# Kernel tuning notes

Hardware: AMD Instinct MI355X
Metric: run time of the kernel (lower is better)

## Reference

```python
import jax, jax.numpy as jnp
import numpy as np

B, N, C, H = 2, 2048, 768, 12
HD = C // H
SCALE = HD ** -0.5


def setup_inputs() -> dict:
    key = jax.random.key(0)
    k1, k2, k3, k4 = jax.random.split(key, 4)
    return {
        "x": jax.random.normal(k1, (B, N, C), dtype=jnp.float32),
        "qkv_w": jax.random.normal(k2, (3 * C, C), dtype=jnp.float32) * (C ** -0.5),
        "proj_w": jax.random.normal(k3, (C, C), dtype=jnp.float32) * (C ** -0.5),
        "proj_b": jax.random.normal(k4, (C,), dtype=jnp.float32) * 0.01,
    }


def reference(x, qkv_w, proj_w, proj_b):
    b, n, c = x.shape
    # qkv: Linear(dim, 3*dim, bias=False) -> (B,N,3,H,HD) -> per-tensor (B,H,N,HD)
    qkv = (x @ qkv_w.T).reshape(b, n, 3, H, HD)
    q, k, v = jnp.moveaxis(qkv, 2, 0)          # each (B,N,H,HD)
    q = q.transpose(0, 2, 1, 3)                # (B,H,N,HD)
    k = k.transpose(0, 2, 1, 3)
    v = v.transpose(0, 2, 1, 3)
    attn_logits = jnp.einsum("bhqd,bhkd->bhqk", q, k) * SCALE  # (B,H,N,N)
    attn = jax.nn.softmax(attn_logits, axis=-1)
    score = jnp.mean(attn, axis=1)             # (B,N,N) mean over heads
    # dropout p=0.0 -> identity
    out = jnp.einsum("bhqk,bhkd->bhqd", attn, v)  # (B,H,N,HD)
    out = out.transpose(0, 2, 1, 3).reshape(b, n, c)
    out = out @ proj_w.T + proj_b
    return out, score
```

## Files before the change

kernel.cpp:

```cpp
#include <hip/hip_runtime.h>
#include <cstddef>

typedef __attribute__((ext_vector_type(8))) short bf16x8;
typedef __attribute__((ext_vector_type(4))) float f32x4;

constexpr int Bb = 2, Nn = 2048, Cc = 768, Hh = 12, HDd = 64;
constexpr float QSCALE = 0.125f * 1.44269504088896340736f;

#define VMCNT(n) asm volatile("s_waitcnt vmcnt(" #n ")" ::: "memory")
#define SBAR() __builtin_amdgcn_s_barrier()

__device__ inline short f2bf(float f) {
  unsigned u = __builtin_bit_cast(unsigned, f);
  u += 0x7fff + ((u >> 16) & 1);
  return (short)(u >> 16);
}
__device__ inline unsigned cvtpk(float a, float b) {
  unsigned r;
  asm("v_cvt_pk_bf16_f32 %0, %1, %2" : "=v"(r) : "v"(a), "v"(b));
  return r;
}
__device__ inline void gl_lds16(const void* g, void* l) {
  __builtin_amdgcn_global_load_lds(
      (const __attribute__((address_space(1))) unsigned*)g,
      (__attribute__((address_space(3))) unsigned*)l, 16, 0, 0);
}
__device__ inline bf16x8 lds8(const short* p) { return *(const bf16x8*)p; }
__device__ inline bf16x8 ld_frag(const short* base, int row, int ch) {
  return *(const bf16x8*)&base[row * 64 + (((ch ^ (row & 7)) << 3))];
}

__global__ __launch_bounds__(256) void cvt_kernel(const float* __restrict__ s,
                                                  short* __restrict__ d) {
  const int i = (blockIdx.x * 256 + threadIdx.x) * 4;
  const float4 v = *(const float4*)&s[i];
  short4 o;
  o.x = f2bf(v.x); o.y = f2bf(v.y); o.z = f2bf(v.z); o.w = f2bf(v.w);
  *(short4*)&d[i] = o;
}

__global__ __launch_bounds__(256) void qkv_mfma(
    const short* __restrict__ A, const short* __restrict__ W,
    short* __restrict__ Qg, short* __restrict__ Kg, short* __restrict__ Vtg) {
  __shared__ short As[2 * 8192];
  __shared__ short Bs[2 * 8192];
  const int t = threadIdx.x, l = t & 63, w = t >> 6;
  const int lr = l & 15, lh = l >> 4;
  const int m0 = blockIdx.x * 128, r0 = blockIdx.y * 128;
  const int wr = w >> 1, wc = w & 1;
  f32x4 acc[4][4];
#pragma unroll
  for (int i = 0; i < 4; ++i)
#pragma unroll
    for (int j = 0; j < 4; ++j) acc[i][j] = (f32x4){0.f, 0.f, 0.f, 0.f};

  auto stage = [&](const int buf, const int kt) {
#pragma unroll
    for (int u = 0; u < 4; ++u) {
      const int du = (w * 4 + u) * 64 + l;
      const int row = du >> 3, ch = du & 7, sch = ch ^ (row & 7);
      gl_lds16(A + (size_t)(m0 + row) * Cc + kt * 64 + sch * 8,
               &As[buf * 8192 + (w * 4 + u) * 512]);
      gl_lds16(W + (size_t)(r0 + row) * Cc + kt * 64 + sch * 8,
               &Bs[buf * 8192 + (w * 4 + u) * 512]);
    }
  };
  auto compute = [&](const int buf) {
    const short* Ab = As + buf * 8192;
    const short* Bbp = Bs + buf * 8192;
#pragma unroll
    for (int kp = 0; kp < 2; ++kp) {
      bf16x8 af[4], bfv[4];
#pragma unroll
      for (int i = 0; i < 4; ++i)
        af[i] = ld_frag(Ab, wr * 64 + i * 16 + lr, kp * 4 + lh);
#pragma unroll
      for (int j = 0; j < 4; ++j)
        bfv[j] = ld_frag(Bbp, wc * 64 + j * 16 + lr, kp * 4 + lh);
      __builtin_amdgcn_s_setprio(1);
#pragma unroll
      for (int i = 0; i < 4; ++i)
#pragma unroll
        for (int j = 0; j < 4; ++j)
          acc[i][j] = __builtin_amdgcn_mfma_f32_16x16x32_bf16(
              af[i], bfv[j], acc[i][j], 0, 0, 0);
      __builtin_amdgcn_s_setprio(0);
    }
  };

  stage(0, 0);
#pragma unroll 1
  for (int kk = 0; kk < 10; kk += 2) {
    stage(1, kk + 1);
    VMCNT(8); SBAR();
    compute(0);
    SBAR();
    stage(0, kk + 2);
    VMCNT(8); SBAR();
    compute(1);
    SBAR();
  }
  stage(1, 11);
  VMCNT(8); SBAR();
  compute(0);
  SBAR();
  VMCNT(0); SBAR();
  compute(1);

  const int which = r0 / Cc;
  const int rbase = r0 % Cc;
  const int bq = m0 >> 11;
  const int nb = (m0 & 2047) + wr * 64;
  if (which == 2) {
#pragma unroll
    for (int j = 0; j < 4; ++j) {
      const int rr = rbase + wc * 64 + j * 16 + lr;
      const int head = rr >> 6, dd = rr & 63;
      short* vp = &Vtg[(((size_t)bq * Hh + head) * HDd + dd) * Nn];
#pragma unroll
      for (int i = 0; i < 4; ++i) {
        short4 o;
        o.x = f2bf(acc[i][j][0]); o.y = f2bf(acc[i][j][1]);
        o.z = f2bf(acc[i][j][2]); o.w = f2bf(acc[i][j][3]);
        *(short4*)&vp[nb + i * 16 + lh * 4] = o;
      }
    }
  } else {
    const float scl = (which == 0) ? QSCALE : 1.0f;
    short* __restrict__ dst = (which == 0) ? Qg : Kg;
#pragma unroll
    for (int j = 0; j < 4; ++j) {
      const int rr = rbase + wc * 64 + j * 16 + lr;
      const int head = rr >> 6, dd = rr & 63;
      short* dp = &dst[((size_t)bq * Hh + head) * Nn * HDd + dd];
#pragma unroll
      for (int i = 0; i < 4; ++i)
#pragma unroll
        for (int r = 0; r < 4; ++r)
          dp[(size_t)(nb + i * 16 + lh * 4 + r) * HDd] =
              f2bf(acc[i][j][r] * scl);
    }
  }
}

__global__ __launch_bounds__(256, 3) void attn_pass1(
    const short* __restrict__ Qg, const short* __restrict__ Kg,
    const short* __restrict__ Vtg, float* __restrict__ Linv,
    short* __restrict__ OHb) {
  __shared__ short SM[4 * 4096 + 4 * 1024];
  const int t = threadIdx.x, l = t & 63, w = t >> 6;
  const int lr = l & 15, lh = l >> 4;
  const int raw = blockIdx.x;
  const int bid = (raw & 7) * 96 + (raw >> 3);
  const int q0 = (bid & 31) * 64;
  const int head = (bid >> 5) % Hh;
  const int b = bid / (32 * Hh);
  const size_t base = (size_t)b * Hh + head;
  const short* Qh = Qg + base * Nn * HDd;
  const short* Kh = Kg + base * Nn * HDd;
  const short* Vh = Vtg + base * HDd * Nn;
  const int qw = q0 + w * 16;
  const int PB = 16384 + w * 1024;

  const bf16x8 onesf = {0x3F80, 0x3F80, 0x3F80, 0x3F80,
                        0x3F80, 0x3F80, 0x3F80, 0x3F80};

  int fof[2][4], wofi[4], pof[2];
#pragma unroll
  for (int kp = 0; kp < 2; ++kp) {
#pragma unroll
    for (int i = 0; i < 4; ++i)
      fof[kp][i] = (i * 16 + lr) * 64 + (((kp * 4 + lh) ^ (lr & 7)) << 3);
    pof[kp] = lr * 64 + (((kp * 4 + lh) ^ (lr & 7)) << 3);
  }
#pragma unroll
  for (int i = 0; i < 4; ++i) {
    const int ch = 2 * i + (lh >> 1);
    wofi[i] = lr * 64 + ((ch ^ (lr & 7)) << 3) + (lh & 1) * 4;
  }

  bf16x8 qf[2];
#pragma unroll
  for (int kp = 0; kp < 2; ++kp)
    qf[kp] = *(const bf16x8*)&Qh[(size_t)(qw + lr) * HDd + kp * 32 + lh * 8];

  f32x4 accO[4], accL;
  accL = (f32x4){0.f, 0.f, 0.f, 0.f};
#pragma unroll
  for (int j = 0; j < 4; ++j) accO[j] = (f32x4){0.f, 0.f, 0.f, 0.f};

  auto stage = [&](const int buf, const int tile) {
    const short* Kt = Kh + (size_t)tile * (64 * HDd);
    const short* Vt = Vh + tile * 64;
#pragma unroll
    for (int u = 0; u < 2; ++u) {
      const int cu = u * 4 + w;
      const int du = cu * 64 + l;
      const int row = du >> 3, ch = du & 7, sch = ch ^ (row & 7);
      gl_lds16(Kt + row * 64 + sch * 8, &SM[buf * 4096 + cu * 512]);
      gl_lds16(Vt + (size_t)row * Nn + sch * 8,
               &SM[8192 + buf * 4096 + cu * 512]);
    }
  };

  auto compute = [&](const int kb) {
    const int vb = 8192 + kb;
    f32x4 sacc[4];
#pragma unroll
    for (int i = 0; i < 4; ++i) sacc[i] = (f32x4){0.f, 0.f, 0.f, 0.f};
    __builtin_amdgcn_s_setprio(1);
#pragma unroll
    for (int kp = 0; kp < 2; ++kp)
#pragma unroll
      for (int i = 0; i < 4; ++i)
        sacc[i] = __builtin_amdgcn_mfma_f32_16x16x32_bf16(
            lds8(&SM[kb + fof[kp][i]]), qf[kp], sacc[i], 0, 0, 0);
    __builtin_amdgcn_s_setprio(0);
#pragma unroll
    for (int i = 0; i < 4; ++i) {
      const float p0 = exp2f(sacc[i][0]), p1 = exp2f(sacc[i][1]);
      const float p2 = exp2f(sacc[i][2]), p3 = exp2f(sacc[i][3]);
      uint2 pk;
      pk.x = cvtpk(p0, p1);
      pk.y = cvtpk(p2, p3);
      *(uint2*)&SM[PB + wofi[i]] = pk;
    }
    __builtin_amdgcn_s_setprio(1);
#pragma unroll
    for (int kp = 0; kp < 2; ++kp) {
      const bf16x8 pa = lds8(&SM[PB + pof[kp]]);
      accL = __builtin_amdgcn_mfma_f32_16x16x32_bf16(pa, onesf, accL, 0, 0, 0);
#pragma unroll
      for (int j = 0; j < 4; ++j)
        accO[j] = __builtin_amdgcn_mfma_f32_16x16x32_bf16(
            pa, lds8(&SM[vb + fof[kp][j]]), accO[j], 0, 0, 0);
    }
    __builtin_amdgcn_s_setprio(0);
  };

  stage(0, 0);
#pragma unroll 1
  for (int it = 0; it < 30; it += 2) {
    stage(1, it + 1);
    VMCNT(4); SBAR();
    compute(0);
    SBAR();
    stage(0, it + 2);
    VMCNT(4); SBAR();
    compute(4096);
    SBAR();
  }
  stage(1, 31);
  VMCNT(4); SBAR();
  compute(0);
  SBAR();
  VMCNT(0); SBAR();
  compute(4096);

  f32x4 linvq;
#pragma unroll
  for (int r = 0; r < 4; ++r) linvq[r] = 1.0f / accL[r];
  if (lr == 0) *(f32x4*)&Linv[base * Nn + qw + 4 * lh] = linvq;
#pragma unroll
  for (int j = 0; j < 4; ++j)
#pragma unroll
    for (int r = 0; r < 4; ++r)
      OHb[((size_t)b * Nn + qw + 4 * lh + r) * Cc + head * HDd + j * 16 + lr] =
          f2bf(accO[j][r] * linvq[r]);
}

__global__ __launch_bounds__(256, 4) void score_mfma(
    const short* __restrict__ Qg, const short* __restrict__ Kg,
    const float* __restrict__ Linv, float* __restrict__ score) {
  __shared__ __align__(16) char SMraw[64 * 68 * 4];
  short* SK = (short*)SMraw;
  float* SMf = (float*)SMraw;
  const int t = threadIdx.x, l = t & 63, w = t >> 6;
  const int lr = l & 15, lh = l >> 4;
  const int raw = blockIdx.x;
  const int xcd = raw & 7, idx = raw >> 3;
  const int b = xcd >> 2;
  const int q0 = ((xcd & 3) * 8 + (idx >> 5)) * 64;
  const int kv0 = (idx & 31) * 64;
  const int qw = q0 + w * 16;

  int fof[2][4];
#pragma unroll
  for (int kp = 0; kp < 2; ++kp)
#pragma unroll
    for (int i = 0; i < 4; ++i)
      fof[kp][i] = (i * 16 + lr) * 64 + (((kp * 4 + lh) ^ (lr & 7)) << 3);

  f32x4 sc[4];
#pragma unroll
  for (int i = 0; i < 4; ++i) sc[i] = (f32x4){0.f, 0.f, 0.f, 0.f};

  auto stage = [&](const int kb, const int h) {
    const short* Kt = Kg + (((size_t)b * Hh + h) * Nn + kv0) * HDd;
#pragma unroll
    for (int u = 0; u < 2; ++u) {
      const int cu = u * 4 + w;
      const int du = cu * 64 + l;
      const int row = du >> 3, ch = du & 7, sch = ch ^ (row & 7);
      gl_lds16(Kt + row * 64 + sch * 8, &SK[kb + cu * 512]);
    }
  };
  auto ldqQ = [&](const int h, bf16x8& a0, bf16x8& a1) {
    const size_t hb = (size_t)b * Hh + h;
    a0 = *(const bf16x8*)&Qg[(hb * Nn + qw + lr) * HDd + lh * 8];
    a1 = *(const bf16x8*)&Qg[(hb * Nn + qw + lr) * HDd + 32 + lh * 8];
  };
  auto qk = [&](const int kb, const bf16x8 a0, const bf16x8 a1,
                f32x4 (&sacc)[4]) {
#pragma unroll
    for (int i = 0; i < 4; ++i) sacc[i] = (f32x4){0.f, 0.f, 0.f, 0.f};
#pragma unroll
    for (int i = 0; i < 4; ++i)
      sacc[i] = __builtin_amdgcn_mfma_f32_16x16x32_bf16(
          lds8(&SK[kb + fof[0][i]]), a0, sacc[i], 0, 0, 0);
#pragma unroll
    for (int i = 0; i < 4; ++i)
      sacc[i] = __builtin_amdgcn_mfma_f32_16x16x32_bf16(
          lds8(&SK[kb + fof[1][i]]), a1, sacc[i], 0, 0, 0);
  };
  auto expacc = [&](const f32x4 (&sacc)[4], const float lv) {
#pragma unroll
    for (int i = 0; i < 4; ++i)
#pragma unroll
      for (int r = 0; r < 4; ++r) sc[i][r] += exp2f(sacc[i][r]) * lv;
  };

  bf16x8 qA0, qA1, qB0, qB1;
  float lvA, lvB;
  f32x4 sA[4], sB[4];
  stage(0, 0);
  ldqQ(0, qA0, qA1);
  __syncthreads();
  stage(4096, 1);
  ldqQ(1, qB0, qB1);
  lvA = Linv[((size_t)b * Hh + 0) * Nn + qw + lr];
  qk(0, qA0, qA1, sA);
  __syncthreads();
#pragma unroll 1
  for (int h = 1; h < 11; h += 2) {
    stage(0, h + 1);
    ldqQ(h + 1, qA0, qA1);
    lvB = Linv[((size_t)b * Hh + h) * Nn + qw + lr];
    qk(4096, qB0, qB1, sB);
    expacc(sA, lvA);
    __syncthreads();
    stage(4096, h + 2);
    ldqQ(h + 2, qB0, qB1);
    lvA = Linv[((size_t)b * Hh + h + 1) * Nn + qw + lr];
    qk(0, qA0, qA1, sA);
    expacc(sB, lvB);
    __syncthreads();
  }
  lvB = Linv[((size_t)b * Hh + 11) * Nn + qw + lr];
  qk(4096, qB0, qB1, sB);
  expacc(sA, lvA);
  expacc(sB, lvB);
  __syncthreads();

  constexpr float invH = 1.0f / 12.0f;
#pragma unroll
  for (int i = 0; i < 4; ++i) {
    f32x4 o;
#pragma unroll
    for (int r = 0; r < 4; ++r) o[r] = sc[i][r] * invH;
    *(f32x4*)&SMf[(w * 16 + lr) * 68 + i * 16 + 4 * lh] = o;
  }
  __syncthreads();
#pragma unroll
  for (int s = 0; s < 4; ++s) {
    const int lin = t + s * 256;
    const int row = lin >> 4, ch = lin & 15;
    const f32x4 v = *(const f32x4*)&SMf[row * 68 + ch * 4];
    *(f32x4*)&score[((size_t)b * Nn + q0 + row) * Nn + kv0 + ch * 4] = v;
  }
}

__global__ __launch_bounds__(256) void proj_mfma(
    const short* __restrict__ A, const short* __restrict__ W,
    const float* __restrict__ bias, float* __restrict__ out) {
  __shared__ short As[128 * 64];
  __shared__ short Bs[128 * 64];
  const int t = threadIdx.x, l = t & 63, w = t >> 6;
  const int lr = l & 15, lh = l >> 4;
  const int m0 = blockIdx.x * 128, c0 = blockIdx.y * 128;
  const int wr = w >> 1, wc = w & 1;
  f32x4 acc[4][4];
#pragma unroll
  for (int i = 0; i < 4; ++i)
#pragma unroll
    for (int j = 0; j < 4; ++j) acc[i][j] = (f32x4){0.f, 0.f, 0.f, 0.f};

  for (int k0 = 0; k0 < Cc; k0 += 64) {
    __syncthreads();
#pragma unroll
    for (int u = 0; u < 4; ++u) {
      const int du = (w * 4 + u) * 64 + l;
      const int row = du >> 3, ch = du & 7, sch = ch ^ (row & 7);
      gl_lds16(A + (size_t)(m0 + row) * Cc + k0 + sch * 8,
               &As[(w * 4 + u) * 512]);
      gl_lds16(W + (size_t)(c0 + row) * Cc + k0 + sch * 8,
               &Bs[(w * 4 + u) * 512]);
    }
    __syncthreads();
#pragma unroll
    for (int kp = 0; kp < 2; ++kp) {
      bf16x8 af[4], bfv[4];
#pragma unroll
      for (int i = 0; i < 4; ++i)
        af[i] = ld_frag(As, wr * 64 + i * 16 + lr, kp * 4 + lh);
#pragma unroll
      for (int j = 0; j < 4; ++j)
        bfv[j] = ld_frag(Bs, wc * 64 + j * 16 + lr, kp * 4 + lh);
#pragma unroll
      for (int i = 0; i < 4; ++i)
#pragma unroll
        for (int j = 0; j < 4; ++j)
          acc[i][j] = __builtin_amdgcn_mfma_f32_16x16x32_bf16(
              af[i], bfv[j], acc[i][j], 0, 0, 0);
    }
  }
#pragma unroll
  for (int j = 0; j < 4; ++j) {
    const int c = c0 + wc * 64 + j * 16 + lr;
    const float bi = bias[c];
#pragma unroll
    for (int i = 0; i < 4; ++i)
#pragma unroll
      for (int r = 0; r < 4; ++r) {
        const int m = m0 + wr * 64 + i * 16 + lh * 4 + r;
        out[(size_t)m * Cc + c] = acc[i][j][r] + bi;
      }
  }
}

extern "C" void kernel_launch(void* const* d_in, const int* in_sizes, int n_in,
                              void* d_out, int out_size, void* d_ws,
                              size_t ws_size, hipStream_t stream) {
  const float* x = (const float*)d_in[0];
  const float* qkv_w = (const float*)d_in[1];
  const float* proj_w = (const float*)d_in[2];
  const float* proj_b = (const float*)d_in[3];

  float* out = (float*)d_out;
  float* score = out + (size_t)Bb * Nn * Cc;

  const size_t nx = (size_t)Bb * Nn * Cc;
  const size_t nwq = (size_t)3 * Cc * Cc;
  const size_t npw = (size_t)Cc * Cc;
  short* xb = (short*)d_ws;
  short* wqb = xb + nx;
  short* pwb = wqb + nwq;
  short* Qb = pwb + npw;
  short* Kb = Qb + nx;
  short* Vtb = Kb + nx;
  short* OHb = Vtb + nx;
  float* Linv = (float*)(OHb + nx);

  cvt_kernel<<<dim3((int)(nx / 1024)), 256, 0, stream>>>(x, xb);
  cvt_kernel<<<dim3((int)(nwq / 1024)), 256, 0, stream>>>(qkv_w, wqb);
  cvt_kernel<<<dim3((int)(npw / 1024)), 256, 0, stream>>>(proj_w, pwb);
  qkv_mfma<<<dim3(32, 18), 256, 0, stream>>>(xb, wqb, Qb, Kb, Vtb);
  attn_pass1<<<dim3(768), 256, 0, stream>>>(Qb, Kb, Vtb, Linv, OHb);
  score_mfma<<<dim3(2048), 256, 0, stream>>>(Qb, Kb, Linv, score);
  proj_mfma<<<dim3(32, 6), 256, 0, stream>>>(OHb, pwb, proj_b, out);
}
```

Before: 141.2 us.

## Merge conversion kernels and retile QKV and projection GEMMs for more blocks

Merges the three fp32-to-bf16 conversion launches into one kernel that picks its source by index, which removes two launches. The QKV GEMM tile goes from 128x128 to 128x96, giving 768 blocks instead of 576, with the staging loop and the wait counts adjusted to match. The projection GEMM tile drops from 128x128 to 64x64 and gains double-buffered LDS staging, raising the block count from 192 to 768 so the GPU's compute units are better filled. Smaller tiles reduce data reuse per block and add redundant global loads.

```diff
diff --git a/kernel.cpp b/kernel.cpp
--- a/kernel.cpp
+++ b/kernel.cpp
@@ -30,10 +30,20 @@
   return *(const bf16x8*)&base[row * 64 + (((ch ^ (row & 7)) << 3))];
 }
 
-__global__ __launch_bounds__(256) void cvt_kernel(const float* __restrict__ s,
-                                                  short* __restrict__ d) {
+__global__ __launch_bounds__(256) void cvt3_kernel(
+    const float* __restrict__ s0, const float* __restrict__ s1,
+    const float* __restrict__ s2, short* __restrict__ d, int n0, int n01) {
   const int i = (blockIdx.x * 256 + threadIdx.x) * 4;
-  const float4 v = *(const float4*)&s[i];
+  const float* src;
+  int off;
+  if (i < n0) {
+    src = s0; off = i;
+  } else if (i < n01) {
+    src = s1; off = i - n0;
+  } else {
+    src = s2; off = i - n01;
+  }
+  const float4 v = *(const float4*)&src[off];
   short4 o;
   o.x = f2bf(v.x); o.y = f2bf(v.y); o.z = f2bf(v.z); o.w = f2bf(v.w);
   *(short4*)&d[i] = o;
@@ -43,45 +53,52 @@
     const short* __restrict__ A, const short* __restrict__ W,
     short* __restrict__ Qg, short* __restrict__ Kg, short* __restrict__ Vtg) {
   __shared__ short As[2 * 8192];
-  __shared__ short Bs[2 * 8192];
+  __shared__ short Bs[2 * 6144];
   const int t = threadIdx.x, l = t & 63, w = t >> 6;
   const int lr = l & 15, lh = l >> 4;
-  const int m0 = blockIdx.x * 128, r0 = blockIdx.y * 128;
+  const int m0 = blockIdx.x * 128, r0 = blockIdx.y * 96;
   const int wr = w >> 1, wc = w & 1;
-  f32x4 acc[4][4];
+  f32x4 acc[4][3];
 #pragma unroll
   for (int i = 0; i < 4; ++i)
 #pragma unroll
-    for (int j = 0; j < 4; ++j) acc[i][j] = (f32x4){0.f, 0.f, 0.f, 0.f};
+    for (int j = 0; j < 3; ++j) acc[i][j] = (f32x4){0.f, 0.f, 0.f, 0.f};
 
   auto stage = [&](const int buf, const int kt) {
 #pragma unroll
     for (int u = 0; u < 4; ++u) {
-      const int du = (w * 4 + u) * 64 + l;
+      const int cu = u * 4 + w;
+      const int du = cu * 64 + l;
       const int row = du >> 3, ch = du & 7, sch = ch ^ (row & 7);
       gl_lds16(A + (size_t)(m0 + row) * Cc + kt * 64 + sch * 8,
-               &As[buf * 8192 + (w * 4 + u) * 512]);
+               &As[buf * 8192 + cu * 512]);
+    }
+#pragma unroll
+    for (int u = 0; u < 3; ++u) {
+      const int cu = u * 4 + w;
+      const int du = cu * 64 + l;
+      const int row = du >> 3, ch = du & 7, sch = ch ^ (row & 7);
       gl_lds16(W + (size_t)(r0 + row) * Cc + kt * 64 + sch * 8,
-               &Bs[buf * 8192 + (w * 4 + u) * 512]);
+               &Bs[buf * 6144 + cu * 512]);
     }
   };
   auto compute = [&](const int buf) {
     const short* Ab = As + buf * 8192;
-    const short* Bbp = Bs + buf * 8192;
+    const short* Bbp = Bs + buf * 6144;
 #pragma unroll
     for (int kp = 0; kp < 2; ++kp) {
-      bf16x8 af[4], bfv[4];
+      bf16x8 af[4], bfv[3];
 #pragma unroll
       for (int i = 0; i < 4; ++i)
         af[i] = ld_frag(Ab, wr * 64 + i * 16 + lr, kp * 4 + lh);
 #pragma unroll
-      for (int j = 0; j < 4; ++j)
-        bfv[j] = ld_frag(Bbp, wc * 64 + j * 16 + lr, kp * 4 + lh);
+      for (int j = 0; j < 3; ++j)
+        bfv[j] = ld_frag(Bbp, wc * 48 + j * 16 + lr, kp * 4 + lh);
       __builtin_amdgcn_s_setprio(1);
 #pragma unroll
       for (int i = 0; i < 4; ++i)
 #pragma unroll
-        for (int j = 0; j < 4; ++j)
+        for (int j = 0; j < 3; ++j)
           acc[i][j] = __builtin_amdgcn_mfma_f32_16x16x32_bf16(
               af[i], bfv[j], acc[i][j], 0, 0, 0);
       __builtin_amdgcn_s_setprio(0);
@@ -92,16 +109,16 @@
 #pragma unroll 1
   for (int kk = 0; kk < 10; kk += 2) {
     stage(1, kk + 1);
-    VMCNT(8); SBAR();
+    VMCNT(7); SBAR();
     compute(0);
     SBAR();
     stage(0, kk + 2);
-    VMCNT(8); SBAR();
+    VMCNT(7); SBAR();
     compute(1);
     SBAR();
   }
   stage(1, 11);
-  VMCNT(8); SBAR();
+  VMCNT(7); SBAR();
   compute(0);
   SBAR();
   VMCNT(0); SBAR();
@@ -113,8 +130,8 @@
   const int nb = (m0 & 2047) + wr * 64;
   if (which == 2) {
 #pragma unroll
-    for (int j = 0; j < 4; ++j) {
-      const int rr = rbase + wc * 64 + j * 16 + lr;
+    for (int j = 0; j < 3; ++j) {
+      const int rr = rbase + wc * 48 + j * 16 + lr;
       const int head = rr >> 6, dd = rr & 63;
       short* vp = &Vtg[(((size_t)bq * Hh + head) * HDd + dd) * Nn];
 #pragma unroll
@@ -129,8 +146,8 @@
     const float scl = (which == 0) ? QSCALE : 1.0f;
     short* __restrict__ dst = (which == 0) ? Qg : Kg;
 #pragma unroll
-    for (int j = 0; j < 4; ++j) {
-      const int rr = rbase + wc * 64 + j * 16 + lr;
+    for (int j = 0; j < 3; ++j) {
+      const int rr = rbase + wc * 48 + j * 16 + lr;
       const int head = rr >> 6, dd = rr & 63;
       short* dp = &dst[((size_t)bq * Hh + head) * Nn * HDd + dd];
 #pragma unroll
@@ -383,56 +400,81 @@
 __global__ __launch_bounds__(256) void proj_mfma(
     const short* __restrict__ A, const short* __restrict__ W,
     const float* __restrict__ bias, float* __restrict__ out) {
-  __shared__ short As[128 * 64];
-  __shared__ short Bs[128 * 64];
+  __shared__ short As[2 * 4096];
+  __shared__ short Bs[2 * 4096];
   const int t = threadIdx.x, l = t & 63, w = t >> 6;
   const int lr = l & 15, lh = l >> 4;
-  const int m0 = blockIdx.x * 128, c0 = blockIdx.y * 128;
+  const int m0 = blockIdx.x * 64, c0 = blockIdx.y * 64;
   const int wr = w >> 1, wc = w & 1;
-  f32x4 acc[4][4];
-#pragma unroll
-  for (int i = 0; i < 4; ++i)
-#pragma unroll
-    for (int j = 0; j < 4; ++j) acc[i][j] = (f32x4){0.f, 0.f, 0.f, 0.f};
-
-  for (int k0 = 0; k0 < Cc; k0 += 64) {
-    __syncthreads();
-#pragma unroll
-    for (int u = 0; u < 4; ++u) {
-      const int du = (w * 4 + u) * 64 + l;
+  f32x4 acc[2][2];
+#pragma unroll
+  for (int i = 0; i < 2; ++i)
+#pragma unroll
+    for (int j = 0; j < 2; ++j) acc[i][j] = (f32x4){0.f, 0.f, 0.f, 0.f};
+
+  auto stage = [&](const int buf, const int kt) {
+#pragma unroll
+    for (int u = 0; u < 2; ++u) {
+      const int cu = u * 4 + w;
+      const int du = cu * 64 + l;
       const int row = du >> 3, ch = du & 7, sch = ch ^ (row & 7);
-      gl_lds16(A + (size_t)(m0 + row) * Cc + k0 + sch * 8,
-               &As[(w * 4 + u) * 512]);
-      gl_lds16(W + (size_t)(c0 + row) * Cc + k0 + sch * 8,
-               &Bs[(w * 4 + u) * 512]);
-    }
-    __syncthreads();
+      gl_lds16(A + (size_t)(m0 + row) * Cc + kt * 64 + sch * 8,
+               &As[buf * 4096 + cu * 512]);
+      gl_lds16(W + (size_t)(c0 + row) * Cc + kt * 64 + sch * 8,
+               &Bs[buf * 4096 + cu * 512]);
+    }
+  };
+  auto compute = [&](const int buf) {
+    const short* Ab = As + buf * 4096;
+    const short* Bbp = Bs + buf * 4096;
 #pragma unroll
     for (int kp = 0; kp < 2; ++kp) {
-      bf16x8 af[4], bfv[4];
-#pragma unroll
-      for (int i = 0; i < 4; ++i)
-        af[i] = ld_frag(As, wr * 64 + i * 16 + lr, kp * 4 + lh);
-#pragma unroll
-      for (int j = 0; j < 4; ++j)
-        bfv[j] = ld_frag(Bs, wc * 64 + j * 16 + lr, kp * 4 + lh);
-#pragma unroll
-      for (int i = 0; i < 4; ++i)
-#pragma unroll
-        for (int j = 0; j < 4; ++j)
+      bf16x8 af[2], bfv[2];
+#pragma unroll
+      for (int i = 0; i < 2; ++i)
+        af[i] = ld_frag(Ab, wr * 32 + i * 16 + lr, kp * 4 + lh);
+#pragma unroll
+      for (int j = 0; j < 2; ++j)
+        bfv[j] = ld_frag(Bbp, wc * 32 + j * 16 + lr, kp * 4 + lh);
+      __builtin_amdgcn_s_setprio(1);
+#pragma unroll
+      for (int i = 0; i < 2; ++i)
+#pragma unroll
+        for (int j = 0; j < 2; ++j)
           acc[i][j] = __builtin_amdgcn_mfma_f32_16x16x32_bf16(
               af[i], bfv[j], acc[i][j], 0, 0, 0);
-    }
-  }
-#pragma unroll
-  for (int j = 0; j < 4; ++j) {
-    const int c = c0 + wc * 64 + j * 16 + lr;
+      __builtin_amdgcn_s_setprio(0);
+    }
+  };
+
+  stage(0, 0);
+#pragma unroll 1
+  for (int kk = 0; kk < 10; kk += 2) {
+    stage(1, kk + 1);
+    VMCNT(4); SBAR();
+    compute(0);
+    SBAR();
+    stage(0, kk + 2);
+    VMCNT(4); SBAR();
+    compute(1);
+    SBAR();
+  }
+  stage(1, 11);
+  VMCNT(4); SBAR();
+  compute(0);
+  SBAR();
+  VMCNT(0); SBAR();
+  compute(1);
+
+#pragma unroll
+  for (int j = 0; j < 2; ++j) {
+    const int c = c0 + wc * 32 + j * 16 + lr;
     const float bi = bias[c];
 #pragma unroll
-    for (int i = 0; i < 4; ++i)
+    for (int i = 0; i < 2; ++i)
 #pragma unroll
       for (int r = 0; r < 4; ++r) {
-        const int m = m0 + wr * 64 + i * 16 + lh * 4 + r;
+        const int m = m0 + wr * 32 + i * 16 + lh * 4 + r;
         out[(size_t)m * Cc + c] = acc[i][j][r] + bi;
       }
   }
@@ -461,11 +503,11 @@
   short* OHb = Vtb + nx;
   float* Linv = (float*)(OHb + nx);
 
-  cvt_kernel<<<dim3((int)(nx / 1024)), 256, 0, stream>>>(x, xb);
-  cvt_kernel<<<dim3((int)(nwq / 1024)), 256, 0, stream>>>(qkv_w, wqb);
-  cvt_kernel<<<dim3((int)(npw / 1024)), 256, 0, stream>>>(proj_w, pwb);
-  qkv_mfma<<<dim3(32, 18), 256, 0, stream>>>(xb, wqb, Qb, Kb, Vtb);
+  const int ncvt = (int)((nx + nwq + npw) / 1024);
+  cvt3_kernel<<<dim3(ncvt), 256, 0, stream>>>(x, qkv_w, proj_w, xb, (int)nx,
+                                              (int)(nx + nwq));
+  qkv_mfma<<<dim3(32, 24), 256, 0, stream>>>(xb, wqb, Qb, Kb, Vtb);
   attn_pass1<<<dim3(768), 256, 0, stream>>>(Qb, Kb, Vtb, Linv, OHb);
   score_mfma<<<dim3(2048), 256, 0, stream>>>(Qb, Kb, Linv, score);
-  proj_mfma<<<dim3(32, 6), 256, 0, stream>>>(OHb, pwb, proj_b, out);
-}
+  proj_mfma<<<dim3(64, 12), 256, 0, stream>>>(OHb, pwb, proj_b, out);
+}
```

New measurement: 125.8 us, median of 3. 10.9% less time.
